# Kernel optimization log

Hardware: AMD Instinct MI355X
Metric: run time of the kernel (lower is better)

The kernel has to match this reference:

```python
import jax, jax.numpy as jnp
import numpy as np

N_NODES = 8192
N_FEATURES = 512
EMB = 128
N_HEADS = 4
EPS = 1e-6


def setup_inputs() -> dict:
    key = jax.random.key(0)
    k1, k2, k3 = jax.random.split(key, 3)
    X = jax.random.normal(k1, (N_NODES, N_FEATURES), dtype=jnp.float32)
    W = jax.random.normal(k2, (N_FEATURES, EMB), dtype=jnp.float32)
    Z = jax.random.normal(k3, (N_HEADS, N_NODES, EMB), dtype=jnp.float32)
    beta = jnp.ones((), dtype=jnp.float32)
    return {"X": X, "W": W, "Z": Z, "beta": beta}


def reference(X, W, Z, beta):
    # DenseLayer: node embedding
    X_emb = X @ W                                   # [N, E]
    # AffinityLayer: Z @ X_emb^T then cosine-style normalization
    aff = jnp.einsum('hne,me->hnm', Z, X_emb)       # [H, N, N]
    X_norm = jnp.linalg.norm(X_emb, axis=-1)        # [N]
    Z_norm = jnp.linalg.norm(Z, axis=-1)            # [H, N]
    aff = aff / (X_norm[None, None, :] + EPS)
    aff = aff / (Z_norm[:, :, None] + EPS)
    # PoolingLayer: max over heads
    aff = jnp.max(aff, axis=0)                      # [N, N]
    # undirected -> symmetrize
    aff = (aff + aff.T) / 2.0
    # ScalingLayer: map [-1,1] -> [0,1]
    aff = (aff + 1.0) / 2.0
    # ExponentiationLayer
    aff = jnp.power(aff, beta)
    return aff
```

## Files before the change

kernel.cpp:

```cpp
#include <hip/hip_runtime.h>
#include <stdint.h>
#include <stddef.h>

#define N_NODES 8192
#define N_FEAT  512
#define EMB     128
#define N_HEADS 4
#define BT      128
#define TG      (N_NODES / BT)
#define NPAIR   (TG * (TG + 1) / 2)

typedef __attribute__((ext_vector_type(8)))  short bf16x8;
typedef __attribute__((ext_vector_type(16))) float f32x16;

__device__ __forceinline__ unsigned short f2bf(float f) {
  union { float f; unsigned int u; } x; x.f = f;
  unsigned int r = (x.u + 0x7FFFu + ((x.u >> 16) & 1u)) >> 16;
  return (unsigned short)r;
}

__device__ __forceinline__ size_t frag_flat(int n, int k) {
  return ((size_t)(((n >> 6) * 2 + ((n >> 5) & 1)) * 8 + (k >> 4)) * 64
          + ((((k >> 3) & 1) << 5) | (n & 31))) * 8 + (k & 7);
}

__device__ __forceinline__ int tidx(int r, int c) {
  return r * 128 + (c ^ (r & 31));
}

__global__ void __launch_bounds__(512) xw_kernel(const float* __restrict__ X,
                                                 const float* __restrict__ W,
                                                 unsigned short* __restrict__ Xf) {
  __shared__ float xs[32][N_FEAT];
  const int t = threadIdx.x;
  const int row0 = blockIdx.x * 32;
#pragma unroll
  for (int i = 0; i < 8; ++i) {
    int e4 = i * 512 + t;
    int row = e4 >> 7;
    int col = (e4 & 127) * 4;
    *(float4*)&xs[row][col] = *(const float4*)&X[(size_t)(row0 + row) * N_FEAT + col];
  }
  __syncthreads();
  const int c0 = (t & 31) * 4;
  const int r0 = (t >> 5) * 2;
  float a00=0.f,a01=0.f,a02=0.f,a03=0.f,a10=0.f,a11=0.f,a12=0.f,a13=0.f;
  for (int k = 0; k < N_FEAT; k += 2) {
    float4 w0 = *(const float4*)&W[(size_t)k * EMB + c0];
    float4 w1 = *(const float4*)&W[(size_t)(k + 1) * EMB + c0];
    float x00 = xs[r0][k],     x01 = xs[r0][k + 1];
    float x10 = xs[r0 + 1][k], x11 = xs[r0 + 1][k + 1];
    a00 += x00*w0.x; a01 += x00*w0.y; a02 += x00*w0.z; a03 += x00*w0.w;
    a10 += x10*w0.x; a11 += x10*w0.y; a12 += x10*w0.z; a13 += x10*w0.w;
    a00 += x01*w1.x; a01 += x01*w1.y; a02 += x01*w1.z; a03 += x01*w1.w;
    a10 += x11*w1.x; a11 += x11*w1.y; a12 += x11*w1.z; a13 += x11*w1.w;
  }
  float s0 = a00*a00 + a01*a01 + a02*a02 + a03*a03;
  float s1 = a10*a10 + a11*a11 + a12*a12 + a13*a13;
#pragma unroll
  for (int off = 16; off >= 1; off >>= 1) {
    s0 += __shfl_xor(s0, off);
    s1 += __shfl_xor(s1, off);
  }
  float inv0 = 1.0f / (sqrtf(s0) + 1e-6f);
  float inv1 = 1.0f / (sqrtf(s1) + 1e-6f);
  union { unsigned short u[4]; uint2 v; } o0, o1;
  o0.u[0]=f2bf(a00*inv0); o0.u[1]=f2bf(a01*inv0); o0.u[2]=f2bf(a02*inv0); o0.u[3]=f2bf(a03*inv0);
  o1.u[0]=f2bf(a10*inv1); o1.u[1]=f2bf(a11*inv1); o1.u[2]=f2bf(a12*inv1); o1.u[3]=f2bf(a13*inv1);
  int n0 = row0 + r0;
  *(uint2*)&Xf[frag_flat(n0, c0)] = o0.v;
  *(uint2*)&Xf[frag_flat(n0 + 1, c0)] = o1.v;
}

__global__ void __launch_bounds__(256) znorm_kernel(const float* __restrict__ in,
                                                    unsigned short* __restrict__ Zf) {
  const int row = blockIdx.x * 4 + (threadIdx.x >> 6);
  const int lane = threadIdx.x & 63;
  float2 v = *(const float2*)&in[(size_t)row * EMB + lane * 2];
  float ss = v.x * v.x + v.y * v.y;
#pragma unroll
  for (int off = 32; off >= 1; off >>= 1) ss += __shfl_xor(ss, off);
  const float s = 1.0f / (sqrtf(ss) + 1e-6f);
  union { unsigned short u[2]; unsigned int w; } o;
  o.u[0] = f2bf(v.x * s);
  o.u[1] = f2bf(v.y * s);
  const int h = row >> 13;
  const int n = row & 8191;
  const int c = lane * 2;
  size_t flat = ((size_t)h << 20) + frag_flat(n, c);
  *(unsigned int*)&Zf[flat] = o.w;
}

__device__ __forceinline__ void aload(bf16x8 (&DST)[8],
                                      const unsigned short* __restrict__ base, int lo) {
#pragma unroll
  for (int kk = 0; kk < 8; ++kk) DST[kk] = *(const bf16x8*)&base[kk * 512 + lo];
}

__device__ __forceinline__ void mstep(const bf16x8 (&CUR)[8],
                                      const bf16x8 (&XB0)[8], const bf16x8 (&XB1)[8],
                                      f32x16& m0, f32x16& m1) {
  f32x16 acc0 = {}, acc1 = {};
#pragma unroll
  for (int kk = 0; kk < 8; ++kk) {
    acc0 = __builtin_amdgcn_mfma_f32_32x32x16_bf16(CUR[kk], XB0[kk], acc0, 0, 0, 0);
    acc1 = __builtin_amdgcn_mfma_f32_32x32x16_bf16(CUR[kk], XB1[kk], acc1, 0, 0, 0);
  }
#pragma unroll
  for (int q = 0; q < 16; ++q) {
    m0[q] = fmaxf(m0[q], acc0[q]);
    m1[q] = fmaxf(m1[q], acc1[q]);
  }
}

__global__ void __launch_bounds__(512) __attribute__((amdgpu_waves_per_eu(2)))
affinity_kernel(const unsigned short* __restrict__ Xf,
                const unsigned short* __restrict__ Zf,
                const float* __restrict__ betap,
                float* __restrict__ out) {
  __shared__ float Tb[BT * BT];

  int bid = blockIdx.x;
  int p = (bid & 7) * (NPAIR / 8) + (bid >> 3);

  int bi, bj;
  {
    int rem = p, Bi = 0, Bj = 0;
    for (Bi = 0; Bi < 4; ++Bi) {
      bool done = false;
      for (Bj = Bi; Bj < 4; ++Bj) {
        int cnt = (Bi == Bj) ? 136 : 256;
        if (rem < cnt) { done = true; break; }
        rem -= cnt;
      }
      if (done) break;
    }
    int li, lj;
    if (Bi == Bj) {
      li = 0;
      while (rem >= 16 - li) { rem -= 16 - li; ++li; }
      lj = li + rem;
    } else {
      li = rem >> 4;
      lj = rem & 15;
    }
    bi = Bi * 16 + li;
    bj = Bj * 16 + lj;
  }
  const bool diag = (bi == bj);

  const int t = threadIdx.x;
  const int lane = t & 63;
  const int wid = t >> 6;
  const int rb = wid >> 1;
  const int cb = wid & 1;
  const int R0 = rb * 32, C0 = cb * 64;
  const int fr = lane & 31, fh = lane >> 5;
  const int lo = lane * 8;

  const size_t HS = (size_t)1 << 20;
  const size_t aI = (size_t)(bi * 4 + rb) << 12;
  const size_t aJ = (size_t)(bj * 4 + rb) << 12;
  const size_t bJ = (size_t)(bj * 4 + cb * 2) << 12;
  const size_t bI = (size_t)(bi * 4 + cb * 2) << 12;

  bf16x8 XB0[8], XB1[8], Aa[8], Ab[8];
  f32x16 m0, m1;

  aload(XB0, Xf + bJ, lo);
  aload(XB1, Xf + bJ + 4096, lo);
  aload(Aa, Zf + aI, lo);
#pragma unroll
  for (int q = 0; q < 16; ++q) { m0[q] = -3.0e38f; m1[q] = -3.0e38f; }

  aload(Ab, Zf + HS + aI, lo);      mstep(Aa, XB0, XB1, m0, m1);
  aload(Aa, Zf + 2 * HS + aI, lo);  mstep(Ab, XB0, XB1, m0, m1);
  aload(Ab, Zf + 3 * HS + aI, lo);  mstep(Aa, XB0, XB1, m0, m1);
                                    mstep(Ab, XB0, XB1, m0, m1);

#pragma unroll
  for (int q = 0; q < 16; ++q) {
    int r = R0 + (q & 3) + 8 * (q >> 2) + 4 * fh;
    Tb[tidx(C0 + fr, r)]      = m0[q];
    Tb[tidx(C0 + 32 + fr, r)] = m1[q];
  }
  __syncthreads();

  const float beta = betap[0];
  const bool bp = (beta != 1.0f);

  if (diag) {
#pragma unroll
    for (int q = 0; q < 16; ++q) {
      int r = R0 + (q & 3) + 8 * (q >> 2) + 4 * fh;
      {
        int c = C0 + fr;
        float v = 0.25f * (m0[q] + Tb[tidx(r, c)]) + 0.5f;
        if (bp) v = powf(v, beta);
        out[(size_t)(bi * BT + r) * N_NODES + (size_t)(bi * BT + c)] = v;
      }
      {
        int c = C0 + 32 + fr;
        float v = 0.25f * (m1[q] + Tb[tidx(r, c)]) + 0.5f;
        if (bp) v = powf(v, beta);
        out[(size_t)(bi * BT + r) * N_NODES + (size_t)(bi * BT + c)] = v;
      }
    }
    return;
  }

  aload(XB0, Xf + bI, lo);
  aload(XB1, Xf + bI + 4096, lo);
  aload(Aa, Zf + aJ, lo);
#pragma unroll
  for (int q = 0; q < 16; ++q) { m0[q] = -3.0e38f; m1[q] = -3.0e38f; }

  aload(Ab, Zf + HS + aJ, lo);      mstep(Aa, XB0, XB1, m0, m1);
  aload(Aa, Zf + 2 * HS + aJ, lo);  mstep(Ab, XB0, XB1, m0, m1);
  aload(Ab, Zf + 3 * HS + aJ, lo);  mstep(Aa, XB0, XB1, m0, m1);
                                    mstep(Ab, XB0, XB1, m0, m1);

  float vv[2][16];
#pragma unroll
  for (int q = 0; q < 16; ++q) {
    int r = R0 + (q & 3) + 8 * (q >> 2) + 4 * fh;
    {
      int c = C0 + fr;
      float v = 0.25f * (m0[q] + Tb[tidx(r, c)]) + 0.5f;
      if (bp) v = powf(v, beta);
      out[(size_t)(bj * BT + r) * N_NODES + (size_t)(bi * BT + c)] = v;
      vv[0][q] = v;
    }
    {
      int c = C0 + 32 + fr;
      float v = 0.25f * (m1[q] + Tb[tidx(r, c)]) + 0.5f;
      if (bp) v = powf(v, beta);
      out[(size_t)(bj * BT + r) * N_NODES + (size_t)(bi * BT + c)] = v;
      vv[1][q] = v;
    }
  }

  __syncthreads();
#pragma unroll
  for (int q = 0; q < 16; ++q) {
    int r = R0 + (q & 3) + 8 * (q >> 2) + 4 * fh;
    Tb[tidx(C0 + fr, r)]      = vv[0][q];
    Tb[tidx(C0 + 32 + fr, r)] = vv[1][q];
  }
  __syncthreads();
#pragma unroll
  for (int it = 0; it < 32; ++it) {
    int row = it * 4 + (t >> 7);
    int col = t & 127;
    out[(size_t)(bi * BT + row) * N_NODES + (size_t)(bj * BT + col)] =
        Tb[tidx(row, col)];
  }
}

extern "C" void kernel_launch(void* const* d_in, const int* in_sizes, int n_in,
                              void* d_out, int out_size, void* d_ws, size_t ws_size,
                              hipStream_t stream) {
  const float* X = (const float*)d_in[0];
  const float* W = (const float*)d_in[1];
  const float* Z = (const float*)d_in[2];
  const float* beta = (const float*)d_in[3];
  float* out = (float*)d_out;
  char* ws = (char*)d_ws;

  unsigned short* Xf = (unsigned short*)ws;
  unsigned short* Zf = (unsigned short*)(ws + (2u << 20));

  hipLaunchKernelGGL(xw_kernel, dim3(N_NODES / 32), dim3(512), 0, stream, X, W, Xf);
  hipLaunchKernelGGL(znorm_kernel, dim3(N_HEADS * N_NODES / 4), dim3(256), 0, stream, Z, Zf);
  hipLaunchKernelGGL(affinity_kernel, dim3(NPAIR), dim3(512), 0, stream, Xf, Zf, beta, out);
}
```

Before: 188.0 us.

## Restructure affinity kernel to 16x16 MFMA with LDS-staged A tiles and bf16 transpose

Rewrites the affinity kernel to use 256 threads, each wave computing a 64x64 subtile with 16x16x32 bf16 MFMAs. The A operand (Z or X rows) is staged through double-buffered LDS using global_load_lds, while B stays in registers. The fragment layout changes to match the new MFMA shape. The transpose buffer is stored as bf16, which halves LDS use but loses precision on the mirrored output half. This aims to raise data reuse per wave and overlap loads with compute, at the cost of a barrier per k-step.

```diff
diff --git a/kernel.cpp b/kernel.cpp
--- a/kernel.cpp
+++ b/kernel.cpp
@@ -10,21 +10,31 @@
 #define TG      (N_NODES / BT)
 #define NPAIR   (TG * (TG + 1) / 2)
 
-typedef __attribute__((ext_vector_type(8)))  short bf16x8;
-typedef __attribute__((ext_vector_type(16))) float f32x16;
+typedef __attribute__((ext_vector_type(8))) short bf16x8;
+typedef __attribute__((ext_vector_type(4))) float f32x4;
 
 __device__ __forceinline__ unsigned short f2bf(float f) {
   union { float f; unsigned int u; } x; x.f = f;
   unsigned int r = (x.u + 0x7FFFu + ((x.u >> 16) & 1u)) >> 16;
   return (unsigned short)r;
 }
-
-__device__ __forceinline__ size_t frag_flat(int n, int k) {
-  return ((size_t)(((n >> 6) * 2 + ((n >> 5) & 1)) * 8 + (k >> 4)) * 64
-          + ((((k >> 3) & 1) << 5) | (n & 31))) * 8 + (k & 7);
-}
-
-__device__ __forceinline__ int tidx(int r, int c) {
+__device__ __forceinline__ float bf2f(unsigned short u) {
+  union { unsigned int u; float f; } x; x.u = ((unsigned int)u) << 16;
+  return x.f;
+}
+
+__device__ __forceinline__ void gl_lds16(const unsigned short* g, unsigned short* l) {
+  __builtin_amdgcn_global_load_lds(
+      (__attribute__((address_space(1))) void*)(void*)g,
+      (__attribute__((address_space(3))) void*)l, 16, 0, 0);
+}
+
+__device__ __forceinline__ size_t frag16(int n, int k) {
+  return ((size_t)((n >> 4) * 4 + (k >> 5)) * 64
+          + ((((k >> 3) & 3) << 4) | (n & 15))) * 8 + (k & 7);
+}
+
+__device__ __forceinline__ int tix(int r, int c) {
   return r * 128 + (c ^ (r & 31));
 }
 
@@ -68,8 +78,8 @@
   o0.u[0]=f2bf(a00*inv0); o0.u[1]=f2bf(a01*inv0); o0.u[2]=f2bf(a02*inv0); o0.u[3]=f2bf(a03*inv0);
   o1.u[0]=f2bf(a10*inv1); o1.u[1]=f2bf(a11*inv1); o1.u[2]=f2bf(a12*inv1); o1.u[3]=f2bf(a13*inv1);
   int n0 = row0 + r0;
-  *(uint2*)&Xf[frag_flat(n0, c0)] = o0.v;
-  *(uint2*)&Xf[frag_flat(n0 + 1, c0)] = o1.v;
+  *(uint2*)&Xf[frag16(n0, c0)] = o0.v;
+  *(uint2*)&Xf[frag16(n0 + 1, c0)] = o1.v;
 }
 
 __global__ void __launch_bounds__(256) znorm_kernel(const float* __restrict__ in,
@@ -87,42 +97,32 @@
   const int h = row >> 13;
   const int n = row & 8191;
   const int c = lane * 2;
-  size_t flat = ((size_t)h << 20) + frag_flat(n, c);
-  *(unsigned int*)&Zf[flat] = o.w;
-}
-
-__device__ __forceinline__ void aload(bf16x8 (&DST)[8],
-                                      const unsigned short* __restrict__ base, int lo) {
-#pragma unroll
-  for (int kk = 0; kk < 8; ++kk) DST[kk] = *(const bf16x8*)&base[kk * 512 + lo];
-}
-
-__device__ __forceinline__ void mstep(const bf16x8 (&CUR)[8],
-                                      const bf16x8 (&XB0)[8], const bf16x8 (&XB1)[8],
-                                      f32x16& m0, f32x16& m1) {
-  f32x16 acc0 = {}, acc1 = {};
-#pragma unroll
-  for (int kk = 0; kk < 8; ++kk) {
-    acc0 = __builtin_amdgcn_mfma_f32_32x32x16_bf16(CUR[kk], XB0[kk], acc0, 0, 0, 0);
-    acc1 = __builtin_amdgcn_mfma_f32_32x32x16_bf16(CUR[kk], XB1[kk], acc1, 0, 0, 0);
-  }
-#pragma unroll
-  for (int q = 0; q < 16; ++q) {
-    m0[q] = fmaxf(m0[q], acc0[q]);
-    m1[q] = fmaxf(m1[q], acc1[q]);
-  }
-}
-
-__global__ void __launch_bounds__(512) __attribute__((amdgpu_waves_per_eu(2)))
+  *(unsigned int*)&Zf[((size_t)h << 20) + frag16(n, c)] = o.w;
+}
+
+__device__ __forceinline__ void stageA(unsigned short* dst,
+                                       const unsigned short* __restrict__ src16,
+                                       int ks, int w, int lane) {
+#pragma unroll
+  for (int i = 0; i < 2; ++i) {
+    int slot = w * 128 + i * 64 + lane;
+    int row = slot >> 2, cq = slot & 3;
+    const unsigned short* g = src16 + ((size_t)((row >> 4) * 4 + ks)) * 512
+                              + (((cq << 4) | (row & 15)) * 8);
+    gl_lds16(g, dst + (size_t)(w * 128 + i * 64) * 8);
+  }
+}
+
+__global__ void __launch_bounds__(256)
 affinity_kernel(const unsigned short* __restrict__ Xf,
                 const unsigned short* __restrict__ Zf,
                 const float* __restrict__ betap,
                 float* __restrict__ out) {
-  __shared__ float Tb[BT * BT];
+  __shared__ __align__(16) unsigned short Asl[2][128 * 32];
+  __shared__ unsigned short Tb[BT * BT];
 
   int bid = blockIdx.x;
   int p = (bid & 7) * (NPAIR / 8) + (bid >> 3);
-
   int bi, bj;
   {
     int rem = p, Bi = 0, Bj = 0;
@@ -151,109 +151,186 @@
 
   const int t = threadIdx.x;
   const int lane = t & 63;
-  const int wid = t >> 6;
-  const int rb = wid >> 1;
-  const int cb = wid & 1;
-  const int R0 = rb * 32, C0 = cb * 64;
-  const int fr = lane & 31, fh = lane >> 5;
-  const int lo = lane * 8;
+  const int w = t >> 6;
+  const int R0 = (w >> 1) * 64;
+  const int C0 = (w & 1) * 64;
+  const int fcol = lane & 15;
+  const int fkq = lane >> 4;
 
   const size_t HS = (size_t)1 << 20;
-  const size_t aI = (size_t)(bi * 4 + rb) << 12;
-  const size_t aJ = (size_t)(bj * 4 + rb) << 12;
-  const size_t bJ = (size_t)(bj * 4 + cb * 2) << 12;
-  const size_t bI = (size_t)(bi * 4 + cb * 2) << 12;
-
-  bf16x8 XB0[8], XB1[8], Aa[8], Ab[8];
-  f32x16 m0, m1;
-
-  aload(XB0, Xf + bJ, lo);
-  aload(XB1, Xf + bJ + 4096, lo);
-  aload(Aa, Zf + aI, lo);
-#pragma unroll
-  for (int q = 0; q < 16; ++q) { m0[q] = -3.0e38f; m1[q] = -3.0e38f; }
-
-  aload(Ab, Zf + HS + aI, lo);      mstep(Aa, XB0, XB1, m0, m1);
-  aload(Aa, Zf + 2 * HS + aI, lo);  mstep(Ab, XB0, XB1, m0, m1);
-  aload(Ab, Zf + 3 * HS + aI, lo);  mstep(Aa, XB0, XB1, m0, m1);
-                                    mstep(Ab, XB0, XB1, m0, m1);
-
-#pragma unroll
-  for (int q = 0; q < 16; ++q) {
-    int r = R0 + (q & 3) + 8 * (q >> 2) + 4 * fh;
-    Tb[tidx(C0 + fr, r)]      = m0[q];
-    Tb[tidx(C0 + 32 + fr, r)] = m1[q];
-  }
+  const unsigned short* ZIbase = Zf + (size_t)(bi * 8) * 2048;
+  const unsigned short* XIbase = Xf + (size_t)(bi * 8) * 2048;
+  const unsigned short* BJbase = Xf + (size_t)(bj * 8 + (C0 >> 4)) * 2048;
+  const unsigned short* BZbase = Zf + (size_t)(bj * 8 + (C0 >> 4)) * 2048;
+
+  bf16x8 B[4][4];
+  f32x4 acc[4][4], m[4][4];
+
+#pragma unroll
+  for (int ks = 0; ks < 4; ++ks)
+#pragma unroll
+    for (int ct = 0; ct < 4; ++ct)
+      B[ks][ct] = *(const bf16x8*)&BJbase[(size_t)ct * 2048 + ks * 512 + lane * 8];
+
+#pragma unroll
+  for (int rt = 0; rt < 4; ++rt)
+#pragma unroll
+    for (int ct = 0; ct < 4; ++ct) {
+      acc[rt][ct] = (f32x4){0.f, 0.f, 0.f, 0.f};
+      m[rt][ct] = (f32x4){-3.0e38f, -3.0e38f, -3.0e38f, -3.0e38f};
+    }
+
+  stageA(Asl[0], ZIbase, 0, w, lane);
   __syncthreads();
+
+#pragma unroll
+  for (int h = 0; h < N_HEADS; ++h) {
+#pragma unroll
+    for (int ks = 0; ks < 4; ++ks) {
+      const int s = h * 4 + ks;
+      const int cur = s & 1;
+      if (s < 15) {
+        const int ns = s + 1;
+        stageA(Asl[ns & 1], ZIbase + (size_t)(ns >> 2) * HS, ns & 3, w, lane);
+      } else if (!diag) {
+        stageA(Asl[(s + 1) & 1], XIbase, 0, w, lane);
+      }
+      bf16x8 a[4];
+#pragma unroll
+      for (int rt = 0; rt < 4; ++rt)
+        a[rt] = *(const bf16x8*)&Asl[cur][(R0 + rt * 16 + fcol) * 32 + (fkq << 3)];
+#pragma unroll
+      for (int rt = 0; rt < 4; ++rt)
+#pragma unroll
+        for (int ct = 0; ct < 4; ++ct)
+          acc[rt][ct] = __builtin_amdgcn_mfma_f32_16x16x32_bf16(a[rt], B[ks][ct],
+                                                                acc[rt][ct], 0, 0, 0);
+      if (ks == 3) {
+#pragma unroll
+        for (int rt = 0; rt < 4; ++rt)
+#pragma unroll
+          for (int ct = 0; ct < 4; ++ct)
+#pragma unroll
+            for (int q = 0; q < 4; ++q) {
+              m[rt][ct][q] = fmaxf(m[rt][ct][q], acc[rt][ct][q]);
+              acc[rt][ct][q] = 0.f;
+            }
+      }
+      __syncthreads();
+    }
+  }
+
+#pragma unroll
+  for (int rt = 0; rt < 4; ++rt)
+#pragma unroll
+    for (int ct = 0; ct < 4; ++ct)
+#pragma unroll
+      for (int q = 0; q < 4; ++q) {
+        int r = R0 + rt * 16 + fkq * 4 + q;
+        int c = C0 + ct * 16 + fcol;
+        Tb[tix(r, c)] = f2bf(m[rt][ct][q]);
+      }
 
   const float beta = betap[0];
   const bool bp = (beta != 1.0f);
 
   if (diag) {
-#pragma unroll
-    for (int q = 0; q < 16; ++q) {
-      int r = R0 + (q & 3) + 8 * (q >> 2) + 4 * fh;
-      {
-        int c = C0 + fr;
-        float v = 0.25f * (m0[q] + Tb[tidx(r, c)]) + 0.5f;
+    __syncthreads();
+#pragma unroll
+    for (int rt = 0; rt < 4; ++rt)
+#pragma unroll
+      for (int ct = 0; ct < 4; ++ct)
+#pragma unroll
+        for (int q = 0; q < 4; ++q) {
+          int r = R0 + rt * 16 + fkq * 4 + q;
+          int c = C0 + ct * 16 + fcol;
+          float v = 0.25f * (m[rt][ct][q] + bf2f(Tb[tix(c, r)])) + 0.5f;
+          if (bp) v = powf(v, beta);
+          out[(size_t)(bi * BT + r) * N_NODES + (size_t)(bi * BT + c)] = v;
+        }
+    return;
+  }
+
+#pragma unroll
+  for (int rt = 0; rt < 4; ++rt)
+#pragma unroll
+    for (int ct = 0; ct < 4; ++ct)
+      m[rt][ct] = (f32x4){-3.0e38f, -3.0e38f, -3.0e38f, -3.0e38f};
+
+#pragma unroll
+  for (int h = 0; h < N_HEADS; ++h) {
+#pragma unroll
+    for (int ks = 0; ks < 4; ++ks)
+#pragma unroll
+      for (int ct = 0; ct < 4; ++ct)
+        B[ks][ct] = *(const bf16x8*)&BZbase[(size_t)h * HS + (size_t)ct * 2048
+                                            + ks * 512 + lane * 8];
+#pragma unroll
+    for (int ks = 0; ks < 4; ++ks) {
+      const int s = h * 4 + ks;
+      const int cur = s & 1;
+      if (s < 15) {
+        stageA(Asl[(s + 1) & 1], XIbase, (s + 1) & 3, w, lane);
+      }
+      bf16x8 a[4];
+#pragma unroll
+      for (int rt = 0; rt < 4; ++rt)
+        a[rt] = *(const bf16x8*)&Asl[cur][(R0 + rt * 16 + fcol) * 32 + (fkq << 3)];
+#pragma unroll
+      for (int rt = 0; rt < 4; ++rt)
+#pragma unroll
+        for (int ct = 0; ct < 4; ++ct)
+          acc[rt][ct] = __builtin_amdgcn_mfma_f32_16x16x32_bf16(a[rt], B[ks][ct],
+                                                                acc[rt][ct], 0, 0, 0);
+      if (ks == 3) {
+#pragma unroll
+        for (int rt = 0; rt < 4; ++rt)
+#pragma unroll
+          for (int ct = 0; ct < 4; ++ct)
+#pragma unroll
+            for (int q = 0; q < 4; ++q) {
+              m[rt][ct][q] = fmaxf(m[rt][ct][q], acc[rt][ct][q]);
+              acc[rt][ct][q] = 0.f;
+            }
+      }
+      __syncthreads();
+    }
+  }
+
+  float vv[4][4][4];
+#pragma unroll
+  for (int rt = 0; rt < 4; ++rt)
+#pragma unroll
+    for (int ct = 0; ct < 4; ++ct)
+#pragma unroll
+      for (int q = 0; q < 4; ++q) {
+        int r = R0 + rt * 16 + fkq * 4 + q;
+        int c = C0 + ct * 16 + fcol;
+        float a = bf2f(Tb[tix(r, c)]);
+        float v = 0.25f * (a + m[rt][ct][q]) + 0.5f;
         if (bp) v = powf(v, beta);
-        out[(size_t)(bi * BT + r) * N_NODES + (size_t)(bi * BT + c)] = v;
-      }
-      {
-        int c = C0 + 32 + fr;
-        float v = 0.25f * (m1[q] + Tb[tidx(r, c)]) + 0.5f;
-        if (bp) v = powf(v, beta);
-        out[(size_t)(bi * BT + r) * N_NODES + (size_t)(bi * BT + c)] = v;
-      }
-    }
-    return;
-  }
-
-  aload(XB0, Xf + bI, lo);
-  aload(XB1, Xf + bI + 4096, lo);
-  aload(Aa, Zf + aJ, lo);
-#pragma unroll
-  for (int q = 0; q < 16; ++q) { m0[q] = -3.0e38f; m1[q] = -3.0e38f; }
-
-  aload(Ab, Zf + HS + aJ, lo);      mstep(Aa, XB0, XB1, m0, m1);
-  aload(Aa, Zf + 2 * HS + aJ, lo);  mstep(Ab, XB0, XB1, m0, m1);
-  aload(Ab, Zf + 3 * HS + aJ, lo);  mstep(Aa, XB0, XB1, m0, m1);
-                                    mstep(Ab, XB0, XB1, m0, m1);
-
-  float vv[2][16];
-#pragma unroll
-  for (int q = 0; q < 16; ++q) {
-    int r = R0 + (q & 3) + 8 * (q >> 2) + 4 * fh;
-    {
-      int c = C0 + fr;
-      float v = 0.25f * (m0[q] + Tb[tidx(r, c)]) + 0.5f;
-      if (bp) v = powf(v, beta);
-      out[(size_t)(bj * BT + r) * N_NODES + (size_t)(bi * BT + c)] = v;
-      vv[0][q] = v;
-    }
-    {
-      int c = C0 + 32 + fr;
-      float v = 0.25f * (m1[q] + Tb[tidx(r, c)]) + 0.5f;
-      if (bp) v = powf(v, beta);
-      out[(size_t)(bj * BT + r) * N_NODES + (size_t)(bi * BT + c)] = v;
-      vv[1][q] = v;
-    }
-  }
+        out[(size_t)(bi * BT + r) * N_NODES + (size_t)(bj * BT + c)] = v;
+        vv[rt][ct][q] = v;
+      }
 
   __syncthreads();
 #pragma unroll
-  for (int q = 0; q < 16; ++q) {
-    int r = R0 + (q & 3) + 8 * (q >> 2) + 4 * fh;
-    Tb[tidx(C0 + fr, r)]      = vv[0][q];
-    Tb[tidx(C0 + 32 + fr, r)] = vv[1][q];
-  }
+  for (int rt = 0; rt < 4; ++rt)
+#pragma unroll
+    for (int ct = 0; ct < 4; ++ct)
+#pragma unroll
+      for (int q = 0; q < 4; ++q) {
+        int r = R0 + rt * 16 + fkq * 4 + q;
+        int c = C0 + ct * 16 + fcol;
+        Tb[tix(c, r)] = f2bf(vv[rt][ct][q]);
+      }
   __syncthreads();
 #pragma unroll
-  for (int it = 0; it < 32; ++it) {
-    int row = it * 4 + (t >> 7);
+  for (int it = 0; it < 64; ++it) {
+    int row = it * 2 + (t >> 7);
     int col = t & 127;
-    out[(size_t)(bi * BT + row) * N_NODES + (size_t)(bj * BT + col)] =
-        Tb[tidx(row, col)];
+    out[(size_t)(bj * BT + row) * N_NODES + (size_t)(bi * BT + col)] =
+        bf2f(Tb[tix(row, col)]);
   }
 }
 
@@ -272,5 +349,5 @@
 
   hipLaunchKernelGGL(xw_kernel, dim3(N_NODES / 32), dim3(512), 0, stream, X, W, Xf);
   hipLaunchKernelGGL(znorm_kernel, dim3(N_HEADS * N_NODES / 4), dim3(256), 0, stream, Z, Zf);
-  hipLaunchKernelGGL(affinity_kernel, dim3(NPAIR), dim3(512), 0, stream, Xf, Zf, beta, out);
-}
+  hipLaunchKernelGGL(affinity_kernel, dim3(NPAIR), dim3(256), 0, stream, Xf, Zf, beta, out);
+}
```

Measured after the change: 323.8 us. +72.2%, slower.
